# Optimization experiments

Measured on AMD Instinct MI355X. Metric: run time of the kernel, lower is better.

The kernel has to match this reference:

```python
import jax, jax.numpy as jnp
import numpy as np

B, T, C = 1, 2048, 1024
H, HKV, DH, WIN = 16, 4, 64, 128
EPS = 1e-5


def rotate_half(x):
    x1, x2 = jnp.split(x, 2, axis=-1)
    return jnp.concatenate((-x2, x1), axis=-1)


def setup_inputs() -> dict:
    key = jax.random.key(0)
    ks = jax.random.split(key, 8)
    s = 0.02
    return {
        "x": jax.random.normal(ks[0], (B, T, C), dtype=jnp.float32),
        "Wq": jax.random.normal(ks[1], (C, H * DH), dtype=jnp.float32) * s,
        "Wk": jax.random.normal(ks[2], (C, HKV * DH), dtype=jnp.float32) * s,
        "Wv": jax.random.normal(ks[3], (C, HKV * DH), dtype=jnp.float32) * s,
        "Wc": jax.random.normal(ks[4], (C, C), dtype=jnp.float32) * s,
        "Wg": jax.random.normal(ks[5], (C, H), dtype=jnp.float32) * s,
        "bg": jax.random.normal(ks[6], (H,), dtype=jnp.float32) * s,
        "rms_w": jnp.ones((C,), dtype=jnp.float32),
    }


def reference(x, Wq, Wk, Wv, Wc, Wg, bg, rms_w):
    n_rep = H // HKV
    # projections -> [B, heads, T, DH]
    q = (x @ Wq).reshape(B, T, H, DH).transpose(0, 2, 1, 3)
    k = (x @ Wk).reshape(B, T, HKV, DH).transpose(0, 2, 1, 3)
    v = (x @ Wv).reshape(B, T, HKV, DH).transpose(0, 2, 1, 3)
    # rotary embedding (freqs duplicated across the two halves)
    inv_freq = 1.0 / (10000.0 ** (jnp.arange(0, DH, 2, dtype=jnp.float32) / DH))
    freqs = jnp.arange(T, dtype=jnp.float32)[:, None] * inv_freq[None, :]
    emb = jnp.concatenate((freqs, freqs), axis=-1)  # [T, DH]
    cos, sin = jnp.cos(emb)[None, None], jnp.sin(emb)[None, None]
    q = q * cos + rotate_half(q) * sin
    k = k * cos + rotate_half(k) * sin
    # GQA: repeat kv heads (contiguous repeat matches torch expand+reshape)
    k = jnp.repeat(k, n_rep, axis=1)
    v = jnp.repeat(v, n_rep, axis=1)
    # gated decay
    gate_logits = (x @ Wg + bg).reshape(B, T, H, 1).transpose(0, 2, 1, 3)  # [B,H,T,1]
    log_alpha = jax.nn.log_sigmoid(gate_logits)
    log_in_scale = jax.nn.log_sigmoid(-gate_logits)
    k_scaled = k * jnp.exp(log_in_scale)
    la_cum = jnp.cumsum(log_alpha, axis=2)                  # [B,H,T,1]
    log_decay = la_cum - jnp.swapaxes(la_cum, 2, 3)         # [B,H,T,T]
    causal = jnp.triu(jnp.ones((T, T), dtype=bool), k=1)
    decay = jnp.exp(jnp.where(causal, -jnp.inf, log_decay))
    scores = jnp.einsum('bhtd,bhsd->bhts', q, k_scaled)
    y_global = jnp.einsum('bhts,bhsd->bhtd', scores * decay, v)
    nb = T // WIN
    qb = q.reshape(B, H, nb, WIN, DH)
    kb = k.reshape(B, H, nb, WIN, DH)
    vb = v.reshape(B, H, nb, WIN, DH)
    att = jnp.einsum('bhnqd,bhnkd->bhnqk', qb, kb) / jnp.sqrt(jnp.float32(DH))
    wmask = jnp.triu(jnp.ones((WIN, WIN), dtype=bool), k=1)
    att = jax.nn.softmax(jnp.where(wmask, -jnp.inf, att), axis=-1)
    y_local = jnp.einsum('bhnqk,bhnkd->bhnqd', att, vb).reshape(B, H, T, DH)
    # fuse, RMSNorm, output projection
    y = (y_global + y_local).transpose(0, 2, 1, 3).reshape(B, T, C)
    y = y * jax.lax.rsqrt(jnp.mean(y * y, axis=-1, keepdims=True) + EPS) * rms_w
    return y @ Wc
```

## Files before the change

### kernel.cpp

```cpp
#include <hip/hip_runtime.h>
#include <hip/hip_bf16.h>


typedef __attribute__((ext_vector_type(8))) short bf16x8;
typedef __attribute__((ext_vector_type(4))) float f32x4;

#define MFMA16(a, b, c) __builtin_amdgcn_mfma_f32_16x16x32_bf16(a, b, c, 0, 0, 0)
#define LN10000_OVER_32 0.28782313662425575f

__device__ __forceinline__ short f2b(float f) {
  __hip_bfloat16 h = __float2bfloat16(f);
  return *reinterpret_cast<short*>(&h);
}
__device__ __forceinline__ float b2f(short s) {
  return __uint_as_float(((unsigned)(unsigned short)s) << 16);
}
__device__ __forceinline__ void gload16(const void* g, void* l) {
  __builtin_amdgcn_global_load_lds(
      (const __attribute__((address_space(1))) void*)g,
      (__attribute__((address_space(3))) void*)l, 16, 0, 0);
}

__device__ __forceinline__ void transpose_cvt_body(
    const float* __restrict__ src, short* __restrict__ dst, int R, int C,
    int bx, int by, float* ts , const float* __restrict__ sw) {
  int c0 = bx * 32, r0 = by * 32;
  int tr = threadIdx.x >> 3, tc = (threadIdx.x & 7) * 4;
  float4 v = *(const float4*)&src[(size_t)(r0 + tr) * C + c0 + tc];
  ts[tr * 33 + tc] = v.x;
  ts[tr * 33 + tc + 1] = v.y;
  ts[tr * 33 + tc + 2] = v.z;
  ts[tr * 33 + tc + 3] = v.w;
  __syncthreads();
  alignas(8) short o[4];
#pragma unroll
  for (int i = 0; i < 4; ++i) {
    float m = sw ? sw[r0 + tc + i] : 1.0f;
    o[i] = f2b(ts[(tc + i) * 33 + tr] * m);
  }
  *(uint2*)&dst[(size_t)(c0 + tr) * R + r0 + tc] = *(uint2*)o;
}

__global__ __launch_bounds__(256) void prep_fused(
    const float* __restrict__ x, const float* __restrict__ Wq,
    const float* __restrict__ Wk, const float* __restrict__ Wv,
    const float* __restrict__ Wc, const float* __restrict__ Wg,
    const float* __restrict__ bg, const float* __restrict__ rmsw,
    short* __restrict__ xb, short* __restrict__ wqkvT,
    short* __restrict__ wcT, float* __restrict__ g, float* __restrict__ rs) {
  __shared__ float ts[32 * 33];
  const int j = blockIdx.x;
  const int tid = threadIdx.x;
  if (j < 2048) {
    const int t = j;
    const int h = tid & 15, chunk = tid >> 4;
    const float* xr = x + (size_t)t * 1024 + chunk * 64;
    const float* wg = Wg + (size_t)chunk * 64 * 16 + h;
    float acc = 0.f;
#pragma unroll
    for (int c = 0; c < 64; c += 4) {
      float4 xv = *(const float4*)(xr + c);
      acc = fmaf(xv.x, wg[(c + 0) * 16], acc);
      acc = fmaf(xv.y, wg[(c + 1) * 16], acc);
      acc = fmaf(xv.z, wg[(c + 2) * 16], acc);
      acc = fmaf(xv.w, wg[(c + 3) * 16], acc);
    }
    ts[chunk * 16 + h] = acc;
    __syncthreads();
    if (tid < 16) {
      float s = bg[tid];
#pragma unroll
      for (int i = 0; i < 16; ++i) s += ts[i * 16 + tid];
      g[t * 16 + tid] = s;
    }
  } else if (j < 3072) {
    int i = ((j - 2048) * 256 + tid) * 8;
    float4 a = *(const float4*)(x + i);
    float4 b = *(const float4*)(x + i + 4);
    alignas(16) short o[8] = {f2b(a.x), f2b(a.y), f2b(a.z), f2b(a.w),
                              f2b(b.x), f2b(b.y), f2b(b.z), f2b(b.w)};
    *(float4*)(xb + i) = *(float4*)o;
  } else if (j < 4096) {
    int jj = j - 3072;
    transpose_cvt_body(Wq, wqkvT, 1024, 1024, jj & 31, jj >> 5, ts, nullptr);
  } else if (j < 4352) {
    int jj = j - 4096;
    transpose_cvt_body(Wk, wqkvT + 1024 * 1024, 1024, 256, jj & 7, jj >> 3, ts,
                       nullptr);
  } else if (j < 4608) {
    int jj = j - 4352;
    transpose_cvt_body(Wv, wqkvT + 1280 * 1024, 1024, 256, jj & 7, jj >> 3, ts,
                       nullptr);
  } else if (j < 5632) {
    int jj = j - 4608;
    transpose_cvt_body(Wc, wcT, 1024, 1024, jj & 31, jj >> 5, ts, rmsw);
  } else {
    int i4 = ((j - 5632) * 256 + tid) * 4;
    float4 z = {0.f, 0.f, 0.f, 0.f};
    *(float4*)(rs + i4) = z;
  }
}

__global__ __launch_bounds__(256) void qkv_gemm_fused(
    const short* __restrict__ A, const short* __restrict__ Bt,
    short* __restrict__ qkvb, short* __restrict__ vtb,
    short* __restrict__ ktb, const float* __restrict__ g,
    float* __restrict__ lac, float* __restrict__ insc) {
  __shared__ short As[128 * 64];
  __shared__ short Bs[64 * 64];
  __shared__ float part[256];
  const int id = blockIdx.x;
  const int tid = threadIdx.x;
  if (id >= 384) {
    const int h = id - 384;
    float vals[8];
    float local = 0.f;
#pragma unroll
    for (int i = 0; i < 8; ++i) {
      int t = tid * 8 + i;
      float gv = g[t * 16 + h];
      float la = (gv > 0.f) ? -log1pf(expf(-gv)) : (gv - log1pf(expf(gv)));
      insc[h * 2048 + t] = 1.f / (1.f + expf(gv));
      vals[i] = la;
      local += la;
    }
    part[tid] = local;
    __syncthreads();
    for (int off = 1; off < 256; off <<= 1) {
      float add = (tid >= off) ? part[tid - off] : 0.f;
      __syncthreads();
      part[tid] += add;
      __syncthreads();
    }
    float run = (tid > 0) ? part[tid - 1] : 0.f;
#pragma unroll
    for (int i = 0; i < 8; ++i) {
      run += vals[i];
      lac[h * 2048 + tid * 8 + i] = run;
    }
    return;
  }
  const int lane = tid & 63, wid = tid >> 6;
  const int l15 = lane & 15, lq = lane >> 4;
  const int jlin = id >> 3;
  const int by = (id & 7) + 8 * (jlin / 24);
  const int bx = jlin % 24;
  const int m0 = by * 128, n0 = bx * 64;
  const int K = 1024;
  const int srow = lane >> 3;
  const int sc16 = (lane & 7) ^ srow;
  f32x4 acc[2][4];
#pragma unroll
  for (int mt = 0; mt < 2; ++mt)
#pragma unroll
    for (int nt = 0; nt < 4; ++nt) acc[mt][nt] = {0.f, 0.f, 0.f, 0.f};
  for (int kt = 0; kt < K; kt += 64) {
    __syncthreads();
#pragma unroll
    for (int i = 0; i < 4; ++i) {
      int jj = wid * 4 + i;
      int row = jj * 8 + srow;
      gload16(A + (size_t)(m0 + row) * K + kt + sc16 * 8, &As[jj * 512]);
    }
#pragma unroll
    for (int i = 0; i < 2; ++i) {
      int jj = wid * 2 + i;
      int row = jj * 8 + srow;
      gload16(Bt + (size_t)(n0 + row) * K + kt + sc16 * 8, &Bs[jj * 512]);
    }
    __syncthreads();
    bf16x8 af[2][2], bfr[4][2];
#pragma unroll
    for (int ks = 0; ks < 2; ++ks) {
      int c16 = ks * 4 + lq;
#pragma unroll
      for (int mt = 0; mt < 2; ++mt) {
        int ar = wid * 32 + mt * 16 + l15;
        af[mt][ks] = *(const bf16x8*)&As[(ar * 8 + (c16 ^ (ar & 7))) * 8];
      }
#pragma unroll
      for (int nt = 0; nt < 4; ++nt) {
        int br = nt * 16 + l15;
        bfr[nt][ks] = *(const bf16x8*)&Bs[(br * 8 + (c16 ^ (br & 7))) * 8];
      }
    }
#pragma unroll
    for (int ks = 0; ks < 2; ++ks)
#pragma unroll
      for (int mt = 0; mt < 2; ++mt)
#pragma unroll
        for (int nt = 0; nt < 4; ++nt)
          acc[mt][nt] = MFMA16(af[mt][ks], bfr[nt][ks], acc[mt][nt]);
  }
  if (bx >= 20) {
#pragma unroll
    for (int mt = 0; mt < 2; ++mt) {
      int row0 = m0 + wid * 32 + mt * 16 + lq * 4;
#pragma unroll
      for (int nt = 0; nt < 4; ++nt) {
        int vcol = (n0 - 1280) + nt * 16 + l15;
        alignas(8) short o4[4];
#pragma unroll
        for (int r = 0; r < 4; ++r) o4[r] = f2b(acc[mt][nt][r]);
        *(uint2*)&vtb[(size_t)vcol * 2048 + row0] = *(uint2*)o4;
      }
    }
    return;
  }
  const bool isk = (bx >= 16);
#pragma unroll
  for (int mt = 0; mt < 2; ++mt) {
    int row0 = m0 + wid * 32 + mt * 16 + lq * 4;
#pragma unroll
    for (int nt = 0; nt < 2; ++nt) {
      int d = nt * 16 + l15;
      float ivf = __expf(-LN10000_OVER_32 * (float)d);
      alignas(8) short oa[4], ob[4];
#pragma unroll
      for (int r = 0; r < 4; ++r) {
        int row_g = row0 + r;
        float th = (float)row_g * ivf;
        float cs = cosf(th), sn = sinf(th);
        float a = acc[mt][nt][r], b = acc[mt][nt + 2][r];
        oa[r] = f2b(a * cs - b * sn);
        ob[r] = f2b(b * cs + a * sn);
        qkvb[(size_t)row_g * 1536 + n0 + d] = oa[r];
        qkvb[(size_t)row_g * 1536 + n0 + d + 32] = ob[r];
      }
      if (isk) {
        int dk = n0 - 1024 + d;
        *(uint2*)&ktb[(size_t)dk * 2048 + row0] = *(uint2*)oa;
        *(uint2*)&ktb[(size_t)(dk + 32) * 2048 + row0] = *(uint2*)ob;
      }
    }
  }
}

__global__ __launch_bounds__(256) void p1_local(
    const short* __restrict__ qkv, const short* __restrict__ vtb,
    const short* __restrict__ ktb, const float* __restrict__ lac,
    const float* __restrict__ insc, float* __restrict__ Bmat,
    short* __restrict__ yl) {
  __shared__ short SA[64 * 64];
  __shared__ short SB[128 * 64];
  __shared__ short SC[64 * 128];
  __shared__ short SD[64 * 128];
  __shared__ float lacs[64], inss[64], gvals[64];
  const int tid = threadIdx.x, lane = tid & 63, wid = tid >> 6;
  const int l15 = lane & 15, lq = lane >> 4;
  const int h = blockIdx.y;
  const int kh = h >> 2;
  if (blockIdx.z == 0) {
    const int c = blockIdx.x;
    short* Ks = SB;
    short* Vts = SC;
    const int srow = lane >> 3;
    const int sc16 = (lane & 7) ^ srow;
#pragma unroll
    for (int i = 0; i < 2; ++i) {
      int jj = wid * 2 + i;
      int row = jj * 8 + srow;
      gload16(ktb + (size_t)(kh * 64 + row) * 2048 + c * 64 + sc16 * 8,
              &Ks[jj * 512]);
      gload16(vtb + (size_t)(kh * 64 + row) * 2048 + c * 64 + sc16 * 8,
              &Vts[jj * 512]);
    }
    if (tid < 64) {
      lacs[tid] = lac[h * 2048 + c * 64 + tid];
      inss[tid] = insc[h * 2048 + c * 64 + tid];
    }
    __syncthreads();
    if (tid < 64)
      gvals[tid] = __expf(fminf(lacs[63] - lacs[tid], 0.f)) * inss[tid];
    __syncthreads();
    const int er = wid * 16 + l15;
    bf16x8 av[2];
#pragma unroll
    for (int ks = 0; ks < 2; ++ks) {
      int c16 = ks * 4 + lq;
      bf16x8 raw = *(const bf16x8*)&Vts[(er * 8 + (c16 ^ (er & 7))) * 8];
      float4 g0 = *(const float4*)&gvals[c16 * 8];
      float4 g1 = *(const float4*)&gvals[c16 * 8 + 4];
      float gv[8] = {g0.x, g0.y, g0.z, g0.w, g1.x, g1.y, g1.z, g1.w};
      bf16x8 sc;
#pragma unroll
      for (int jx = 0; jx < 8; ++jx) sc[jx] = f2b(b2f(raw[jx]) * gv[jx]);
      av[ks] = sc;
    }
    f32x4 acc[4];
#pragma unroll
    for (int nt = 0; nt < 4; ++nt) acc[nt] = {0.f, 0.f, 0.f, 0.f};
#pragma unroll
    for (int ks = 0; ks < 2; ++ks) {
      int c16 = ks * 4 + lq;
#pragma unroll
      for (int nt = 0; nt < 4; ++nt) {
        int dr = nt * 16 + l15;
        bf16x8 bk = *(const bf16x8*)&Ks[(dr * 8 + (c16 ^ (dr & 7))) * 8];
        acc[nt] = MFMA16(av[ks], bk, acc[nt]);
      }
    }
    float* Bout = Bmat + (size_t)(h * 32 + c) * 4096;
#pragma unroll
    for (int nt = 0; nt < 4; ++nt)
#pragma unroll
      for (int r = 0; r < 4; ++r) {
        int e = wid * 16 + lq * 4 + r;
        Bout[e * 64 + nt * 16 + l15] = acc[nt][r];
      }
  } else {
    const int half = blockIdx.x & 1, wb = blockIdx.x >> 1;
    const int t0 = wb * 128;
    short* Qs = SA;
    short* Ks = SB;
    short* Vts = SC;
    short* Ps = SD;
#pragma unroll
    for (int i = 0; i < 2; ++i) {
      int cix = tid + 256 * i;
      int row = cix >> 3, cc = cix & 7;
      *(float4*)&Qs[(row * 8 + (cc ^ (row & 7))) * 8] =
          *(const float4*)&qkv[(size_t)(t0 + half * 64 + row) * 1536 + h * 64 + cc * 8];
    }
#pragma unroll
    for (int i = 0; i < 4; ++i) {
      int cix = tid + 256 * i;
      int row = cix >> 3, cc = cix & 7;
      *(float4*)&Ks[(row * 8 + (cc ^ (row & 7))) * 8] =
          *(const float4*)&qkv[(size_t)(t0 + row) * 1536 + 1024 + kh * 64 + cc * 8];
    }
#pragma unroll
    for (int i = 0; i < 4; ++i) {
      int cix = tid + 256 * i;
      int row = cix >> 4, cc = cix & 15;
      int sw = (row * 16 + ((cc & 8) | ((cc & 7) ^ (row & 7)))) * 8;
      *(float4*)&Vts[sw] =
          *(const float4*)&vtb[(size_t)(kh * 64 + row) * 2048 + t0 + cc * 8];
    }
    __syncthreads();
    const int qr = wid * 16 + l15;
    bf16x8 aq[2];
#pragma unroll
    for (int ks = 0; ks < 2; ++ks) {
      int c16 = ks * 4 + lq;
      aq[ks] = *(const bf16x8*)&Qs[(qr * 8 + (c16 ^ (qr & 7))) * 8];
    }
    f32x4 sv[2][4];
    const int nst = half + 1;
    for (int st = 0; st < nst; ++st)
#pragma unroll
      for (int nt = 0; nt < 4; ++nt) {
        int kr = st * 64 + nt * 16 + l15;
        bf16x8 bk0 = *(const bf16x8*)&Ks[(kr * 8 + ((0 + lq) ^ (kr & 7))) * 8];
        bf16x8 bk1 = *(const bf16x8*)&Ks[(kr * 8 + ((4 + lq) ^ (kr & 7))) * 8];
        f32x4 z = {0.f, 0.f, 0.f, 0.f};
        z = MFMA16(aq[0], bk0, z);
        z = MFMA16(aq[1], bk1, z);
        sv[st][nt] = z;
      }
    float mrow[4], ssum[4];
#pragma unroll
    for (int r = 0; r < 4; ++r) mrow[r] = -1e30f;
    for (int st = 0; st < nst; ++st)
#pragma unroll
      for (int nt = 0; nt < 4; ++nt) {
        int col = st * 64 + nt * 16 + l15;
#pragma unroll
        for (int r = 0; r < 4; ++r) {
          int row = half * 64 + wid * 16 + lq * 4 + r;
          float v = (col <= row) ? sv[st][nt][r] * 0.125f : -1e30f;
          sv[st][nt][r] = v;
          mrow[r] = fmaxf(mrow[r], v);
        }
      }
#pragma unroll
    for (int r = 0; r < 4; ++r) {
      for (int off = 1; off < 16; off <<= 1)
        mrow[r] = fmaxf(mrow[r], __shfl_xor(mrow[r], off, 64));
      ssum[r] = 0.f;
    }
    for (int st = 0; st < nst; ++st)
#pragma unroll
      for (int nt = 0; nt < 4; ++nt) {
        int col = st * 64 + nt * 16 + l15;
#pragma unroll
        for (int r = 0; r < 4; ++r) {
          float e = __expf(sv[st][nt][r] - mrow[r]);
          ssum[r] += e;
          int row = wid * 16 + lq * 4 + r;
          int c16 = col >> 3;
          Ps[(row * 16 + ((c16 & 8) | ((c16 & 7) ^ (row & 7)))) * 8 + (col & 7)] =
              f2b(e);
        }
      }
#pragma unroll
    for (int r = 0; r < 4; ++r) {
      for (int off = 1; off < 16; off <<= 1) ssum[r] += __shfl_xor(ssum[r], off, 64);
      ssum[r] = 1.f / ssum[r];
    }
    __syncthreads();
    f32x4 o[4];
#pragma unroll
    for (int nt = 0; nt < 4; ++nt) o[nt] = {0.f, 0.f, 0.f, 0.f};
    for (int ks = 0; ks < nst * 2; ++ks) {
      int c16 = ks * 4 + lq;
      bf16x8 ap = *(const bf16x8*)&Ps[(qr * 16 + ((c16 & 8) | ((c16 & 7) ^ (qr & 7)))) * 8];
#pragma unroll
      for (int nt = 0; nt < 4; ++nt) {
        int vr = nt * 16 + l15;
        bf16x8 bv = *(const bf16x8*)&Vts[(vr * 16 + ((c16 & 8) | ((c16 & 7) ^ (vr & 7)))) * 8];
        o[nt] = MFMA16(ap, bv, o[nt]);
      }
    }
#pragma unroll
    for (int nt = 0; nt < 4; ++nt)
#pragma unroll
      for (int r = 0; r < 4; ++r) {
        int row_g = t0 + half * 64 + wid * 16 + lq * 4 + r;
        int colg = h * 64 + nt * 16 + l15;
        yl[(size_t)row_g * 1024 + colg] = f2b(o[nt][r] * ssum[r]);
      }
  }
}

__global__ __launch_bounds__(256) void scan_kernel(
    const float* __restrict__ Bmat, const float* __restrict__ lac,
    short* __restrict__ St) {
  const int h = blockIdx.x, tid = threadIdx.x;
  __shared__ float lacE[32];
  if (tid < 32) lacE[tid] = lac[h * 2048 + tid * 64 + 63];
  __syncthreads();
  const int base = tid * 16;
  float S[16];
#pragma unroll
  for (int i = 0; i < 16; ++i) S[i] = 0.f;
  alignas(16) short z16[16];
#pragma unroll
  for (int i = 0; i < 16; ++i) z16[i] = 0;
  *(uint4*)&St[(size_t)(h * 32) * 4096 + base] = *(uint4*)z16;
  *(uint4*)&St[(size_t)(h * 32) * 4096 + base + 8] = *(uint4*)(z16 + 8);
  const float* Bp0 = Bmat + (size_t)(h * 32) * 4096 + base;
  float4 p0 = *(const float4*)(Bp0 + 0);
  float4 p1 = *(const float4*)(Bp0 + 4);
  float4 p2 = *(const float4*)(Bp0 + 8);
  float4 p3 = *(const float4*)(Bp0 + 12);
  for (int c = 1; c < 32; ++c) {
    float4 n0 = p0, n1 = p1, n2 = p2, n3 = p3;
    if (c < 31) {
      const float* Bn = Bmat + (size_t)(h * 32 + c) * 4096 + base;
      n0 = *(const float4*)(Bn + 0);
      n1 = *(const float4*)(Bn + 4);
      n2 = *(const float4*)(Bn + 8);
      n3 = *(const float4*)(Bn + 12);
    }
    float a = (c >= 2) ? __expf(fminf(lacE[c - 1] - lacE[c - 2], 0.f)) : 0.f;
    float bb[16] = {p0.x, p0.y, p0.z, p0.w, p1.x, p1.y, p1.z, p1.w,
                    p2.x, p2.y, p2.z, p2.w, p3.x, p3.y, p3.z, p3.w};
    alignas(16) short o16[16];
#pragma unroll
    for (int i = 0; i < 16; ++i) {
      S[i] = fmaf(a, S[i], bb[i]);
      o16[i] = f2b(S[i]);
    }
    *(uint4*)&St[(size_t)(h * 32 + c) * 4096 + base] = *(uint4*)o16;
    *(uint4*)&St[(size_t)(h * 32 + c) * 4096 + base + 8] = *(uint4*)(o16 + 8);
    p0 = n0; p1 = n1; p2 = n2; p3 = n3;
  }
}

__global__ __launch_bounds__(256) void global_attn_v3(
    const short* __restrict__ qkv, const short* __restrict__ vtb,
    const short* __restrict__ St, const float* __restrict__ lac,
    const float* __restrict__ insc, const short* __restrict__ ylc,
    short* __restrict__ ys, float* __restrict__ rs) {
  const int c = blockIdx.x, h = blockIdx.y;
  const int kh = h >> 2;
  __shared__ short Qs[64 * 64], Ks[64 * 64], Vts[64 * 64], Sts[64 * 64],
      Ps[64 * 64];
  __shared__ float lacq[64], inss[64];
  __shared__ float laprev_sh;
  const int tid = threadIdx.x, lane = tid & 63, wid = tid >> 6;
  const int l15 = lane & 15, lq = lane >> 4;
  const int srow = lane >> 3;
  const int sc16 = (lane & 7) ^ srow;
#pragma unroll
  for (int i = 0; i < 2; ++i) {
    int jj = wid * 2 + i;
    int row = jj * 8 + srow;
    gload16(qkv + (size_t)(c * 64 + row) * 1536 + h * 64 + sc16 * 8,
            &Qs[jj * 512]);
    gload16(qkv + (size_t)(c * 64 + row) * 1536 + 1024 + kh * 64 + sc16 * 8,
            &Ks[jj * 512]);
    gload16(vtb + (size_t)(kh * 64 + row) * 2048 + c * 64 + sc16 * 8,
            &Vts[jj * 512]);
    gload16(St + (size_t)(h * 32 + c) * 4096 + row * 64 + sc16 * 8,
            &Sts[jj * 512]);
  }
  if (tid < 64) {
    lacq[tid] = lac[h * 2048 + c * 64 + tid];
    inss[tid] = insc[h * 2048 + c * 64 + tid];
  }
  if (tid == 0) laprev_sh = (c > 0) ? lac[h * 2048 + c * 64 - 1] : 1e30f;
  __syncthreads();
  const int qr = wid * 16 + l15;
  bf16x8 aq[2];
#pragma unroll
  for (int ks = 0; ks < 2; ++ks) {
    int c16 = ks * 4 + lq;
    aq[ks] = *(const bf16x8*)&Qs[(qr * 8 + (c16 ^ (qr & 7))) * 8];
  }
  f32x4 sv[4];
#pragma unroll
  for (int nt = 0; nt < 4; ++nt) {
    int kr = nt * 16 + l15;
    bf16x8 bk0 = *(const bf16x8*)&Ks[(kr * 8 + ((0 + lq) ^ (kr & 7))) * 8];
    bf16x8 bk1 = *(const bf16x8*)&Ks[(kr * 8 + ((4 + lq) ^ (kr & 7))) * 8];
    f32x4 z = {0.f, 0.f, 0.f, 0.f};
    z = MFMA16(aq[0], bk0, z);
    z = MFMA16(aq[1], bk1, z);
    sv[nt] = z;
  }
#pragma unroll
  for (int nt = 0; nt < 4; ++nt) {
    int col = nt * 16 + l15;
    float ls = lacq[col], is = inss[col];
#pragma unroll
    for (int r = 0; r < 4; ++r) {
      int row = wid * 16 + lq * 4 + r;
      float d = lacq[row] - ls;
      float w = __expf(fminf(d, 0.f)) * is;
      if (col > row) w = 0.f;
      Ps[(row * 8 + ((col >> 3) ^ (row & 7))) * 8 + (col & 7)] = f2b(sv[nt][r] * w);
    }
  }
  f32x4 oi[4];
#pragma unroll
  for (int nt = 0; nt < 4; ++nt) {
    int er = nt * 16 + l15;
    bf16x8 bs0 = *(const bf16x8*)&Sts[(er * 8 + ((0 + lq) ^ (er & 7))) * 8];
    bf16x8 bs1 = *(const bf16x8*)&Sts[(er * 8 + ((4 + lq) ^ (er & 7))) * 8];
    f32x4 z = {0.f, 0.f, 0.f, 0.f};
    z = MFMA16(aq[0], bs0, z);
    z = MFMA16(aq[1], bs1, z);
    oi[nt] = z;
  }
  __syncthreads();
  bf16x8 ap[2];
#pragma unroll
  for (int ks = 0; ks < 2; ++ks) {
    int c16 = ks * 4 + lq;
    ap[ks] = *(const bf16x8*)&Ps[(qr * 8 + (c16 ^ (qr & 7))) * 8];
  }
  f32x4 o[4];
#pragma unroll
  for (int nt = 0; nt < 4; ++nt) {
    int vr = nt * 16 + l15;
    bf16x8 bv0 = *(const bf16x8*)&Vts[(vr * 8 + ((0 + lq) ^ (vr & 7))) * 8];
    bf16x8 bv1 = *(const bf16x8*)&Vts[(vr * 8 + ((4 + lq) ^ (vr & 7))) * 8];
    f32x4 z = {0.f, 0.f, 0.f, 0.f};
    z = MFMA16(ap[0], bv0, z);
    z = MFMA16(ap[1], bv1, z);
    o[nt] = z;
  }
  const float laprev = laprev_sh;
#pragma unroll
  for (int r = 0; r < 4; ++r) {
    int row = wid * 16 + lq * 4 + r;
    float rfac = __expf(fminf(lacq[row] - laprev, 0.f));
    int row_g = c * 64 + row;
    float ssq = 0.f;
#pragma unroll
    for (int nt = 0; nt < 4; ++nt) {
      int colg = h * 64 + nt * 16 + l15;
      size_t idx = (size_t)row_g * 1024 + colg;
      float v = o[nt][r] + rfac * oi[nt][r] + b2f(ylc[idx]);
      ys[idx] = f2b(v);
      ssq = fmaf(v, v, ssq);
    }
    for (int off = 1; off < 16; off <<= 1) ssq += __shfl_xor(ssq, off, 64);
    if (l15 == 0) atomicAdd(&rs[row_g], ssq);
  }
}

__global__ __launch_bounds__(256) void out_gemm(
    const short* __restrict__ A, const short* __restrict__ Bt,
    const float* __restrict__ rs, float* __restrict__ C) {
  __shared__ short As[64 * 64];
  __shared__ short Bs[64 * 64];
  const int tid = threadIdx.x, lane = tid & 63, wid = tid >> 6;
  const int l15 = lane & 15, lq = lane >> 4;
  const int wm = wid >> 1, wn = wid & 1;
  const int id = blockIdx.x;
  const int jlin = id >> 3;
  const int by = (id & 7) + 8 * (jlin / 16);
  const int bx = jlin % 16;
  const int m0 = by * 64, n0 = bx * 64;
  const int K = 1024;
  const int srow = lane >> 3;
  const int sc16 = (lane & 7) ^ srow;
  f32x4 acc[2][2];
#pragma unroll
  for (int mt = 0; mt < 2; ++mt)
#pragma unroll
    for (int nt = 0; nt < 2; ++nt) acc[mt][nt] = {0.f, 0.f, 0.f, 0.f};
  for (int kt = 0; kt < K; kt += 64) {
    __syncthreads();
#pragma unroll
    for (int i = 0; i < 2; ++i) {
      int jj = wid * 2 + i;
      int row = jj * 8 + srow;
      gload16(A + (size_t)(m0 + row) * K + kt + sc16 * 8, &As[jj * 512]);
      gload16(Bt + (size_t)(n0 + row) * K + kt + sc16 * 8, &Bs[jj * 512]);
    }
    __syncthreads();
    bf16x8 af[2][2], bfr[2][2];
#pragma unroll
    for (int ks = 0; ks < 2; ++ks) {
      int c16 = ks * 4 + lq;
#pragma unroll
      for (int mt = 0; mt < 2; ++mt) {
        int ar = wm * 32 + mt * 16 + l15;
        af[mt][ks] = *(const bf16x8*)&As[(ar * 8 + (c16 ^ (ar & 7))) * 8];
      }
#pragma unroll
      for (int nt = 0; nt < 2; ++nt) {
        int br = wn * 32 + nt * 16 + l15;
        bfr[nt][ks] = *(const bf16x8*)&Bs[(br * 8 + (c16 ^ (br & 7))) * 8];
      }
    }
#pragma unroll
    for (int ks = 0; ks < 2; ++ks)
#pragma unroll
      for (int mt = 0; mt < 2; ++mt)
#pragma unroll
        for (int nt = 0; nt < 2; ++nt)
          acc[mt][nt] = MFMA16(af[mt][ks], bfr[nt][ks], acc[mt][nt]);
  }
#pragma unroll
  for (int mt = 0; mt < 2; ++mt) {
    int row0 = m0 + wm * 32 + mt * 16 + lq * 4;
#pragma unroll
    for (int r = 0; r < 4; ++r) {
      int row_g = row0 + r;
      float sc = rsqrtf(rs[row_g] * (1.0f / 1024.0f) + 1e-5f);
#pragma unroll
      for (int nt = 0; nt < 2; ++nt)
        C[(size_t)row_g * 1024 + n0 + wn * 32 + nt * 16 + l15] =
            acc[mt][nt][r] * sc;
    }
  }
}

extern "C" void kernel_launch(void* const* d_in, const int* in_sizes, int n_in,
                              void* d_out, int out_size, void* d_ws,
                              size_t ws_size, hipStream_t stream) {
  const float* x = (const float*)d_in[0];
  const float* Wq = (const float*)d_in[1];
  const float* Wk = (const float*)d_in[2];
  const float* Wv = (const float*)d_in[3];
  const float* Wc = (const float*)d_in[4];
  const float* Wg = (const float*)d_in[5];
  const float* bg = (const float*)d_in[6];
  const float* rmsw = (const float*)d_in[7];
  float* out = (float*)d_out;

  short* wqkvT = (short*)d_ws;
  short* wcT = wqkvT + 1536 * 1024;
  short* qkvb = wcT + 1024 * 1024;
  short* vtb = qkvb + 2048 * 1536;
  short* ktb = vtb + 256 * 2048;
  float* gw = (float*)(ktb + 256 * 2048);
  float* lacw = gw + 2048 * 16;
  float* inscw = lacw + 16 * 2048;
  float* Bmat = inscw + 16 * 2048;
  short* Stb = (short*)(Bmat + 16 * 32 * 4096);
  short* xb = Stb + 16 * 32 * 4096;
  short* ys = xb;
  short* ylc = xb + 2048 * 1024;
  float* rsq = (float*)(ylc + 2048 * 1024);

  prep_fused<<<5634, 256, 0, stream>>>(x, Wq, Wk, Wv, Wc, Wg, bg, rmsw, xb,
                                       wqkvT, wcT, gw, rsq);
  qkv_gemm_fused<<<400, 256, 0, stream>>>(xb, wqkvT, qkvb, vtb, ktb, gw, lacw,
                                          inscw);
  p1_local<<<dim3(32, 16, 2), 256, 0, stream>>>(qkvb, vtb, ktb, lacw, inscw,
                                                Bmat, ylc);
  scan_kernel<<<16, 256, 0, stream>>>(Bmat, lacw, Stb);
  global_attn_v3<<<dim3(32, 16), 256, 0, stream>>>(qkvb, vtb, Stb, lacw, inscw,
                                                   ylc, ys, rsq);
  out_gemm<<<512, 256, 0, stream>>>(ys, wcT, rsq, out);
}
```

Baseline: 150.8 us.

## Fuse local windowed softmax attention into global attention kernel; widen scan parallelism

Result: faster. 133.7 us (-11.3%).

```diff
diff --git a/kernel.cpp b/kernel.cpp
--- a/kernel.cpp
+++ b/kernel.cpp
@@ -236,247 +236,105 @@
   }
 }
 
-__global__ __launch_bounds__(256) void p1_local(
-    const short* __restrict__ qkv, const short* __restrict__ vtb,
-    const short* __restrict__ ktb, const float* __restrict__ lac,
-    const float* __restrict__ insc, float* __restrict__ Bmat,
-    short* __restrict__ yl) {
-  __shared__ short SA[64 * 64];
-  __shared__ short SB[128 * 64];
-  __shared__ short SC[64 * 128];
-  __shared__ short SD[64 * 128];
+__global__ __launch_bounds__(256) void chunk_state(
+    const short* __restrict__ vtb, const short* __restrict__ ktb,
+    const float* __restrict__ lac, const float* __restrict__ insc,
+    float* __restrict__ Bmat) {
+  __shared__ short Ks[64 * 64], Vts[64 * 64];
   __shared__ float lacs[64], inss[64], gvals[64];
   const int tid = threadIdx.x, lane = tid & 63, wid = tid >> 6;
   const int l15 = lane & 15, lq = lane >> 4;
-  const int h = blockIdx.y;
-  const int kh = h >> 2;
-  if (blockIdx.z == 0) {
-    const int c = blockIdx.x;
-    short* Ks = SB;
-    short* Vts = SC;
-    const int srow = lane >> 3;
-    const int sc16 = (lane & 7) ^ srow;
-#pragma unroll
-    for (int i = 0; i < 2; ++i) {
-      int jj = wid * 2 + i;
-      int row = jj * 8 + srow;
-      gload16(ktb + (size_t)(kh * 64 + row) * 2048 + c * 64 + sc16 * 8,
-              &Ks[jj * 512]);
-      gload16(vtb + (size_t)(kh * 64 + row) * 2048 + c * 64 + sc16 * 8,
-              &Vts[jj * 512]);
-    }
-    if (tid < 64) {
-      lacs[tid] = lac[h * 2048 + c * 64 + tid];
-      inss[tid] = insc[h * 2048 + c * 64 + tid];
-    }
-    __syncthreads();
-    if (tid < 64)
-      gvals[tid] = __expf(fminf(lacs[63] - lacs[tid], 0.f)) * inss[tid];
-    __syncthreads();
-    const int er = wid * 16 + l15;
-    bf16x8 av[2];
-#pragma unroll
-    for (int ks = 0; ks < 2; ++ks) {
-      int c16 = ks * 4 + lq;
-      bf16x8 raw = *(const bf16x8*)&Vts[(er * 8 + (c16 ^ (er & 7))) * 8];
-      float4 g0 = *(const float4*)&gvals[c16 * 8];
-      float4 g1 = *(const float4*)&gvals[c16 * 8 + 4];
-      float gv[8] = {g0.x, g0.y, g0.z, g0.w, g1.x, g1.y, g1.z, g1.w};
-      bf16x8 sc;
-#pragma unroll
-      for (int jx = 0; jx < 8; ++jx) sc[jx] = f2b(b2f(raw[jx]) * gv[jx]);
-      av[ks] = sc;
-    }
-    f32x4 acc[4];
-#pragma unroll
-    for (int nt = 0; nt < 4; ++nt) acc[nt] = {0.f, 0.f, 0.f, 0.f};
-#pragma unroll
-    for (int ks = 0; ks < 2; ++ks) {
-      int c16 = ks * 4 + lq;
-#pragma unroll
-      for (int nt = 0; nt < 4; ++nt) {
-        int dr = nt * 16 + l15;
-        bf16x8 bk = *(const bf16x8*)&Ks[(dr * 8 + (c16 ^ (dr & 7))) * 8];
-        acc[nt] = MFMA16(av[ks], bk, acc[nt]);
-      }
-    }
-    float* Bout = Bmat + (size_t)(h * 32 + c) * 4096;
-#pragma unroll
-    for (int nt = 0; nt < 4; ++nt)
-#pragma unroll
-      for (int r = 0; r < 4; ++r) {
-        int e = wid * 16 + lq * 4 + r;
-        Bout[e * 64 + nt * 16 + l15] = acc[nt][r];
-      }
-  } else {
-    const int half = blockIdx.x & 1, wb = blockIdx.x >> 1;
-    const int t0 = wb * 128;
-    short* Qs = SA;
-    short* Ks = SB;
-    short* Vts = SC;
-    short* Ps = SD;
-#pragma unroll
-    for (int i = 0; i < 2; ++i) {
-      int cix = tid + 256 * i;
-      int row = cix >> 3, cc = cix & 7;
-      *(float4*)&Qs[(row * 8 + (cc ^ (row & 7))) * 8] =
-          *(const float4*)&qkv[(size_t)(t0 + half * 64 + row) * 1536 + h * 64 + cc * 8];
-    }
-#pragma unroll
-    for (int i = 0; i < 4; ++i) {
-      int cix = tid + 256 * i;
-      int row = cix >> 3, cc = cix & 7;
-      *(float4*)&Ks[(row * 8 + (cc ^ (row & 7))) * 8] =
-          *(const float4*)&qkv[(size_t)(t0 + row) * 1536 + 1024 + kh * 64 + cc * 8];
-    }
-#pragma unroll
-    for (int i = 0; i < 4; ++i) {
-      int cix = tid + 256 * i;
-      int row = cix >> 4, cc = cix & 15;
-      int sw = (row * 16 + ((cc & 8) | ((cc & 7) ^ (row & 7)))) * 8;
-      *(float4*)&Vts[sw] =
-          *(const float4*)&vtb[(size_t)(kh * 64 + row) * 2048 + t0 + cc * 8];
-    }
-    __syncthreads();
-    const int qr = wid * 16 + l15;
-    bf16x8 aq[2];
-#pragma unroll
-    for (int ks = 0; ks < 2; ++ks) {
-      int c16 = ks * 4 + lq;
-      aq[ks] = *(const bf16x8*)&Qs[(qr * 8 + (c16 ^ (qr & 7))) * 8];
-    }
-    f32x4 sv[2][4];
-    const int nst = half + 1;
-    for (int st = 0; st < nst; ++st)
-#pragma unroll
-      for (int nt = 0; nt < 4; ++nt) {
-        int kr = st * 64 + nt * 16 + l15;
-        bf16x8 bk0 = *(const bf16x8*)&Ks[(kr * 8 + ((0 + lq) ^ (kr & 7))) * 8];
-        bf16x8 bk1 = *(const bf16x8*)&Ks[(kr * 8 + ((4 + lq) ^ (kr & 7))) * 8];
-        f32x4 z = {0.f, 0.f, 0.f, 0.f};
-        z = MFMA16(aq[0], bk0, z);
-        z = MFMA16(aq[1], bk1, z);
-        sv[st][nt] = z;
-      }
-    float mrow[4], ssum[4];
-#pragma unroll
-    for (int r = 0; r < 4; ++r) mrow[r] = -1e30f;
-    for (int st = 0; st < nst; ++st)
-#pragma unroll
-      for (int nt = 0; nt < 4; ++nt) {
-        int col = st * 64 + nt * 16 + l15;
-#pragma unroll
-        for (int r = 0; r < 4; ++r) {
-          int row = half * 64 + wid * 16 + lq * 4 + r;
-          float v = (col <= row) ? sv[st][nt][r] * 0.125f : -1e30f;
-          sv[st][nt][r] = v;
-          mrow[r] = fmaxf(mrow[r], v);
-        }
-      }
+  const int h = blockIdx.y, kh = h >> 2, c = blockIdx.x;
+  const int srow = lane >> 3;
+  const int sc16 = (lane & 7) ^ srow;
+#pragma unroll
+  for (int i = 0; i < 2; ++i) {
+    int jj = wid * 2 + i;
+    int row = jj * 8 + srow;
+    gload16(ktb + (size_t)(kh * 64 + row) * 2048 + c * 64 + sc16 * 8,
+            &Ks[jj * 512]);
+    gload16(vtb + (size_t)(kh * 64 + row) * 2048 + c * 64 + sc16 * 8,
+            &Vts[jj * 512]);
+  }
+  if (tid < 64) {
+    lacs[tid] = lac[h * 2048 + c * 64 + tid];
+    inss[tid] = insc[h * 2048 + c * 64 + tid];
+  }
+  __syncthreads();
+  if (tid < 64)
+    gvals[tid] = __expf(fminf(lacs[63] - lacs[tid], 0.f)) * inss[tid];
+  __syncthreads();
+  const int er = wid * 16 + l15;
+  bf16x8 av[2];
+#pragma unroll
+  for (int ks = 0; ks < 2; ++ks) {
+    int c16 = ks * 4 + lq;
+    bf16x8 raw = *(const bf16x8*)&Vts[(er * 8 + (c16 ^ (er & 7))) * 8];
+    float4 g0 = *(const float4*)&gvals[c16 * 8];
+    float4 g1 = *(const float4*)&gvals[c16 * 8 + 4];
+    float gv[8] = {g0.x, g0.y, g0.z, g0.w, g1.x, g1.y, g1.z, g1.w};
+    bf16x8 sc;
+#pragma unroll
+    for (int jx = 0; jx < 8; ++jx) sc[jx] = f2b(b2f(raw[jx]) * gv[jx]);
+    av[ks] = sc;
+  }
+  f32x4 acc[4];
+#pragma unroll
+  for (int nt = 0; nt < 4; ++nt) acc[nt] = {0.f, 0.f, 0.f, 0.f};
+#pragma unroll
+  for (int ks = 0; ks < 2; ++ks) {
+    int c16 = ks * 4 + lq;
+#pragma unroll
+    for (int nt = 0; nt < 4; ++nt) {
+      int dr = nt * 16 + l15;
+      bf16x8 bk = *(const bf16x8*)&Ks[(dr * 8 + (c16 ^ (dr & 7))) * 8];
+      acc[nt] = MFMA16(av[ks], bk, acc[nt]);
+    }
+  }
+  float* Bout = Bmat + (size_t)(h * 32 + c) * 4096;
+#pragma unroll
+  for (int nt = 0; nt < 4; ++nt)
 #pragma unroll
     for (int r = 0; r < 4; ++r) {
-      for (int off = 1; off < 16; off <<= 1)
-        mrow[r] = fmaxf(mrow[r], __shfl_xor(mrow[r], off, 64));
-      ssum[r] = 0.f;
-    }
-    for (int st = 0; st < nst; ++st)
-#pragma unroll
-      for (int nt = 0; nt < 4; ++nt) {
-        int col = st * 64 + nt * 16 + l15;
-#pragma unroll
-        for (int r = 0; r < 4; ++r) {
-          float e = __expf(sv[st][nt][r] - mrow[r]);
-          ssum[r] += e;
-          int row = wid * 16 + lq * 4 + r;
-          int c16 = col >> 3;
-          Ps[(row * 16 + ((c16 & 8) | ((c16 & 7) ^ (row & 7)))) * 8 + (col & 7)] =
-              f2b(e);
-        }
-      }
-#pragma unroll
-    for (int r = 0; r < 4; ++r) {
-      for (int off = 1; off < 16; off <<= 1) ssum[r] += __shfl_xor(ssum[r], off, 64);
-      ssum[r] = 1.f / ssum[r];
-    }
-    __syncthreads();
-    f32x4 o[4];
-#pragma unroll
-    for (int nt = 0; nt < 4; ++nt) o[nt] = {0.f, 0.f, 0.f, 0.f};
-    for (int ks = 0; ks < nst * 2; ++ks) {
-      int c16 = ks * 4 + lq;
-      bf16x8 ap = *(const bf16x8*)&Ps[(qr * 16 + ((c16 & 8) | ((c16 & 7) ^ (qr & 7)))) * 8];
-#pragma unroll
-      for (int nt = 0; nt < 4; ++nt) {
-        int vr = nt * 16 + l15;
-        bf16x8 bv = *(const bf16x8*)&Vts[(vr * 16 + ((c16 & 8) | ((c16 & 7) ^ (vr & 7)))) * 8];
-        o[nt] = MFMA16(ap, bv, o[nt]);
-      }
-    }
-#pragma unroll
-    for (int nt = 0; nt < 4; ++nt)
-#pragma unroll
-      for (int r = 0; r < 4; ++r) {
-        int row_g = t0 + half * 64 + wid * 16 + lq * 4 + r;
-        int colg = h * 64 + nt * 16 + l15;
-        yl[(size_t)row_g * 1024 + colg] = f2b(o[nt][r] * ssum[r]);
-      }
-  }
+      int e = wid * 16 + lq * 4 + r;
+      Bout[e * 64 + nt * 16 + l15] = acc[nt][r];
+    }
 }
 
 __global__ __launch_bounds__(256) void scan_kernel(
     const float* __restrict__ Bmat, const float* __restrict__ lac,
     short* __restrict__ St) {
-  const int h = blockIdx.x, tid = threadIdx.x;
+  const int h = blockIdx.x, sl = blockIdx.y, tid = threadIdx.x;
   __shared__ float lacE[32];
   if (tid < 32) lacE[tid] = lac[h * 2048 + tid * 64 + 63];
   __syncthreads();
-  const int base = tid * 16;
-  float S[16];
-#pragma unroll
-  for (int i = 0; i < 16; ++i) S[i] = 0.f;
-  alignas(16) short z16[16];
-#pragma unroll
-  for (int i = 0; i < 16; ++i) z16[i] = 0;
-  *(uint4*)&St[(size_t)(h * 32) * 4096 + base] = *(uint4*)z16;
-  *(uint4*)&St[(size_t)(h * 32) * 4096 + base + 8] = *(uint4*)(z16 + 8);
-  const float* Bp0 = Bmat + (size_t)(h * 32) * 4096 + base;
-  float4 p0 = *(const float4*)(Bp0 + 0);
-  float4 p1 = *(const float4*)(Bp0 + 4);
-  float4 p2 = *(const float4*)(Bp0 + 8);
-  float4 p3 = *(const float4*)(Bp0 + 12);
+  const int base = sl * 512 + tid * 2;
+  float S0 = 0.f, S1 = 0.f;
+  *(unsigned*)&St[(size_t)(h * 32) * 4096 + base] = 0u;
+  float2 p = *(const float2*)(Bmat + (size_t)(h * 32) * 4096 + base);
   for (int c = 1; c < 32; ++c) {
-    float4 n0 = p0, n1 = p1, n2 = p2, n3 = p3;
-    if (c < 31) {
-      const float* Bn = Bmat + (size_t)(h * 32 + c) * 4096 + base;
-      n0 = *(const float4*)(Bn + 0);
-      n1 = *(const float4*)(Bn + 4);
-      n2 = *(const float4*)(Bn + 8);
-      n3 = *(const float4*)(Bn + 12);
-    }
+    float2 n = p;
+    if (c < 31) n = *(const float2*)(Bmat + (size_t)(h * 32 + c) * 4096 + base);
     float a = (c >= 2) ? __expf(fminf(lacE[c - 1] - lacE[c - 2], 0.f)) : 0.f;
-    float bb[16] = {p0.x, p0.y, p0.z, p0.w, p1.x, p1.y, p1.z, p1.w,
-                    p2.x, p2.y, p2.z, p2.w, p3.x, p3.y, p3.z, p3.w};
-    alignas(16) short o16[16];
-#pragma unroll
-    for (int i = 0; i < 16; ++i) {
-      S[i] = fmaf(a, S[i], bb[i]);
-      o16[i] = f2b(S[i]);
-    }
-    *(uint4*)&St[(size_t)(h * 32 + c) * 4096 + base] = *(uint4*)o16;
-    *(uint4*)&St[(size_t)(h * 32 + c) * 4096 + base + 8] = *(uint4*)(o16 + 8);
-    p0 = n0; p1 = n1; p2 = n2; p3 = n3;
-  }
-}
-
-__global__ __launch_bounds__(256) void global_attn_v3(
+    S0 = fmaf(a, S0, p.x);
+    S1 = fmaf(a, S1, p.y);
+    unsigned pack = (unsigned)(unsigned short)f2b(S0) |
+                    ((unsigned)(unsigned short)f2b(S1) << 16);
+    *(unsigned*)&St[(size_t)(h * 32 + c) * 4096 + base] = pack;
+    p = n;
+  }
+}
+
+__global__ __launch_bounds__(256) void fused_attn(
     const short* __restrict__ qkv, const short* __restrict__ vtb,
     const short* __restrict__ St, const float* __restrict__ lac,
-    const float* __restrict__ insc, const short* __restrict__ ylc,
-    short* __restrict__ ys, float* __restrict__ rs) {
+    const float* __restrict__ insc, short* __restrict__ ys,
+    float* __restrict__ rs) {
   const int c = blockIdx.x, h = blockIdx.y;
   const int kh = h >> 2;
-  __shared__ short Qs[64 * 64], Ks[64 * 64], Vts[64 * 64], Sts[64 * 64],
-      Ps[64 * 64];
+  const bool odd = (c & 1) != 0;
+  __shared__ short Qs[64 * 64], Kd[64 * 64], Vd[64 * 64], Sts[64 * 64],
+      Kp[64 * 64], Vp[64 * 64], Pd[64 * 64], Pp[64 * 64];
   __shared__ float lacq[64], inss[64];
   __shared__ float laprev_sh;
   const int tid = threadIdx.x, lane = tid & 63, wid = tid >> 6;
@@ -490,11 +348,23 @@
     gload16(qkv + (size_t)(c * 64 + row) * 1536 + h * 64 + sc16 * 8,
             &Qs[jj * 512]);
     gload16(qkv + (size_t)(c * 64 + row) * 1536 + 1024 + kh * 64 + sc16 * 8,
-            &Ks[jj * 512]);
+            &Kd[jj * 512]);
     gload16(vtb + (size_t)(kh * 64 + row) * 2048 + c * 64 + sc16 * 8,
-            &Vts[jj * 512]);
+            &Vd[jj * 512]);
     gload16(St + (size_t)(h * 32 + c) * 4096 + row * 64 + sc16 * 8,
             &Sts[jj * 512]);
+  }
+  if (odd) {
+#pragma unroll
+    for (int i = 0; i < 2; ++i) {
+      int jj = wid * 2 + i;
+      int row = jj * 8 + srow;
+      gload16(qkv + (size_t)((c - 1) * 64 + row) * 1536 + 1024 + kh * 64 +
+                  sc16 * 8,
+              &Kp[jj * 512]);
+      gload16(vtb + (size_t)(kh * 64 + row) * 2048 + (c - 1) * 64 + sc16 * 8,
+              &Vp[jj * 512]);
+    }
   }
   if (tid < 64) {
     lacq[tid] = lac[h * 2048 + c * 64 + tid];
@@ -513,25 +383,28 @@
 #pragma unroll
   for (int nt = 0; nt < 4; ++nt) {
     int kr = nt * 16 + l15;
-    bf16x8 bk0 = *(const bf16x8*)&Ks[(kr * 8 + ((0 + lq) ^ (kr & 7))) * 8];
-    bf16x8 bk1 = *(const bf16x8*)&Ks[(kr * 8 + ((4 + lq) ^ (kr & 7))) * 8];
+    bf16x8 bk0 = *(const bf16x8*)&Kd[(kr * 8 + ((0 + lq) ^ (kr & 7))) * 8];
+    bf16x8 bk1 = *(const bf16x8*)&Kd[(kr * 8 + ((4 + lq) ^ (kr & 7))) * 8];
     f32x4 z = {0.f, 0.f, 0.f, 0.f};
     z = MFMA16(aq[0], bk0, z);
     z = MFMA16(aq[1], bk1, z);
     sv[nt] = z;
   }
-#pragma unroll
-  for (int nt = 0; nt < 4; ++nt) {
-    int col = nt * 16 + l15;
-    float ls = lacq[col], is = inss[col];
-#pragma unroll
-    for (int r = 0; r < 4; ++r) {
-      int row = wid * 16 + lq * 4 + r;
-      float d = lacq[row] - ls;
-      float w = __expf(fminf(d, 0.f)) * is;
-      if (col > row) w = 0.f;
-      Ps[(row * 8 + ((col >> 3) ^ (row & 7))) * 8 + (col & 7)] = f2b(sv[nt][r] * w);
-    }
+  f32x4 sp[4];
+  if (odd) {
+#pragma unroll
+    for (int nt = 0; nt < 4; ++nt) {
+      int kr = nt * 16 + l15;
+      bf16x8 bk0 = *(const bf16x8*)&Kp[(kr * 8 + ((0 + lq) ^ (kr & 7))) * 8];
+      bf16x8 bk1 = *(const bf16x8*)&Kp[(kr * 8 + ((4 + lq) ^ (kr & 7))) * 8];
+      f32x4 z = {0.f, 0.f, 0.f, 0.f};
+      z = MFMA16(aq[0], bk0, z);
+      z = MFMA16(aq[1], bk1, z);
+      sp[nt] = z;
+    }
+  } else {
+#pragma unroll
+    for (int nt = 0; nt < 4; ++nt) sp[nt] = {0.f, 0.f, 0.f, 0.f};
   }
   f32x4 oi[4];
 #pragma unroll
@@ -544,23 +417,100 @@
     z = MFMA16(aq[1], bs1, z);
     oi[nt] = z;
   }
+  float mrow[4], ssum[4];
+  float vd[4][4], vp[4][4];
+#pragma unroll
+  for (int r = 0; r < 4; ++r) mrow[r] = -1e30f;
+#pragma unroll
+  for (int nt = 0; nt < 4; ++nt) {
+    int col = nt * 16 + l15;
+#pragma unroll
+    for (int r = 0; r < 4; ++r) {
+      int row = wid * 16 + lq * 4 + r;
+      float xv = (col <= row) ? sv[nt][r] * 0.125f : -1e30f;
+      vd[nt][r] = xv;
+      mrow[r] = fmaxf(mrow[r], xv);
+      if (odd) {
+        float xp = sp[nt][r] * 0.125f;
+        vp[nt][r] = xp;
+        mrow[r] = fmaxf(mrow[r], xp);
+      }
+    }
+  }
+#pragma unroll
+  for (int r = 0; r < 4; ++r) {
+    for (int off = 1; off < 16; off <<= 1)
+      mrow[r] = fmaxf(mrow[r], __shfl_xor(mrow[r], off, 64));
+    ssum[r] = 0.f;
+  }
+#pragma unroll
+  for (int nt = 0; nt < 4; ++nt) {
+#pragma unroll
+    for (int r = 0; r < 4; ++r) {
+      float e = __expf(vd[nt][r] - mrow[r]);
+      vd[nt][r] = e;
+      ssum[r] += e;
+      if (odd) {
+        float ep = __expf(vp[nt][r] - mrow[r]);
+        vp[nt][r] = ep;
+        ssum[r] += ep;
+      }
+    }
+  }
+#pragma unroll
+  for (int r = 0; r < 4; ++r) {
+    for (int off = 1; off < 16; off <<= 1) ssum[r] += __shfl_xor(ssum[r], off, 64);
+    ssum[r] = 1.f / ssum[r];
+  }
+#pragma unroll
+  for (int nt = 0; nt < 4; ++nt) {
+    int col = nt * 16 + l15;
+    float ls = lacq[col], is = inss[col];
+#pragma unroll
+    for (int r = 0; r < 4; ++r) {
+      int row = wid * 16 + lq * 4 + r;
+      float w = __expf(fminf(lacq[row] - ls, 0.f)) * is;
+      if (col > row) w = 0.f;
+      float pc = sv[nt][r] * w + vd[nt][r] * ssum[r];
+      Pd[(row * 8 + ((col >> 3) ^ (row & 7))) * 8 + (col & 7)] = f2b(pc);
+      if (odd)
+        Pp[(row * 8 + ((col >> 3) ^ (row & 7))) * 8 + (col & 7)] =
+            f2b(vp[nt][r] * ssum[r]);
+    }
+  }
   __syncthreads();
   bf16x8 ap[2];
 #pragma unroll
   for (int ks = 0; ks < 2; ++ks) {
     int c16 = ks * 4 + lq;
-    ap[ks] = *(const bf16x8*)&Ps[(qr * 8 + (c16 ^ (qr & 7))) * 8];
+    ap[ks] = *(const bf16x8*)&Pd[(qr * 8 + (c16 ^ (qr & 7))) * 8];
   }
   f32x4 o[4];
 #pragma unroll
   for (int nt = 0; nt < 4; ++nt) {
     int vr = nt * 16 + l15;
-    bf16x8 bv0 = *(const bf16x8*)&Vts[(vr * 8 + ((0 + lq) ^ (vr & 7))) * 8];
-    bf16x8 bv1 = *(const bf16x8*)&Vts[(vr * 8 + ((4 + lq) ^ (vr & 7))) * 8];
+    bf16x8 bv0 = *(const bf16x8*)&Vd[(vr * 8 + ((0 + lq) ^ (vr & 7))) * 8];
+    bf16x8 bv1 = *(const bf16x8*)&Vd[(vr * 8 + ((4 + lq) ^ (vr & 7))) * 8];
     f32x4 z = {0.f, 0.f, 0.f, 0.f};
     z = MFMA16(ap[0], bv0, z);
     z = MFMA16(ap[1], bv1, z);
     o[nt] = z;
+  }
+  if (odd) {
+    bf16x8 app[2];
+#pragma unroll
+    for (int ks = 0; ks < 2; ++ks) {
+      int c16 = ks * 4 + lq;
+      app[ks] = *(const bf16x8*)&Pp[(qr * 8 + (c16 ^ (qr & 7))) * 8];
+    }
+#pragma unroll
+    for (int nt = 0; nt < 4; ++nt) {
+      int vr = nt * 16 + l15;
+      bf16x8 bv0 = *(const bf16x8*)&Vp[(vr * 8 + ((0 + lq) ^ (vr & 7))) * 8];
+      bf16x8 bv1 = *(const bf16x8*)&Vp[(vr * 8 + ((4 + lq) ^ (vr & 7))) * 8];
+      o[nt] = MFMA16(app[0], bv0, o[nt]);
+      o[nt] = MFMA16(app[1], bv1, o[nt]);
+    }
   }
   const float laprev = laprev_sh;
 #pragma unroll
@@ -573,7 +523,7 @@
     for (int nt = 0; nt < 4; ++nt) {
       int colg = h * 64 + nt * 16 + l15;
       size_t idx = (size_t)row_g * 1024 + colg;
-      float v = o[nt][r] + rfac * oi[nt][r] + b2f(ylc[idx]);
+      float v = o[nt][r] + rfac * oi[nt][r];
       ys[idx] = f2b(v);
       ssq = fmaf(v, v, ssq);
     }
@@ -683,10 +633,9 @@
                                        wqkvT, wcT, gw, rsq);
   qkv_gemm_fused<<<400, 256, 0, stream>>>(xb, wqkvT, qkvb, vtb, ktb, gw, lacw,
                                           inscw);
-  p1_local<<<dim3(32, 16, 2), 256, 0, stream>>>(qkvb, vtb, ktb, lacw, inscw,
-                                                Bmat, ylc);
-  scan_kernel<<<16, 256, 0, stream>>>(Bmat, lacw, Stb);
-  global_attn_v3<<<dim3(32, 16), 256, 0, stream>>>(qkvb, vtb, Stb, lacw, inscw,
-                                                   ylc, ys, rsq);
+  chunk_state<<<dim3(32, 16), 256, 0, stream>>>(vtb, ktb, lacw, inscw, Bmat);
+  scan_kernel<<<dim3(16, 8), 256, 0, stream>>>(Bmat, lacw, Stb);
+  fused_attn<<<dim3(32, 16), 256, 0, stream>>>(qkvb, vtb, Stb, lacw, inscw,
+                                               ys, rsq);
   out_gemm<<<512, 256, 0, stream>>>(ys, wcT, rsq, out);
 }
```
